# Performance work log

Hardware: AMD Instinct MI355X
Metric: run time of the kernel (lower is better)

## Reference

```python
import jax, jax.numpy as jnp
import numpy as np

B, T, D_MODEL, HEADS = 2, 2048, 1024, 16
D_HEAD = D_MODEL // HEADS


def setup_inputs() -> dict:
    key = jax.random.key(0)
    ks = jax.random.split(key, 9)
    s = 1.0 / np.sqrt(D_HEAD)
    return {
        "x": jax.random.normal(ks[0], (B, T, D_MODEL), dtype=jnp.float32),
        "Wq": jax.random.normal(ks[1], (D_HEAD, D_HEAD), dtype=jnp.float32) * s,
        "bq": jax.random.normal(ks[2], (D_HEAD,), dtype=jnp.float32) * 0.01,
        "Wk": jax.random.normal(ks[3], (D_HEAD, D_HEAD), dtype=jnp.float32) * s,
        "bk": jax.random.normal(ks[4], (D_HEAD,), dtype=jnp.float32) * 0.01,
        "Wv": jax.random.normal(ks[5], (D_HEAD, D_HEAD), dtype=jnp.float32) * s,
        "bv": jax.random.normal(ks[6], (D_HEAD,), dtype=jnp.float32) * 0.01,
        "Wp": jax.random.normal(ks[7], (D_MODEL, D_MODEL), dtype=jnp.float32) * (1.0 / np.sqrt(D_MODEL)),
        "bp": jax.random.normal(ks[8], (D_MODEL,), dtype=jnp.float32) * 0.01,
    }


def reference(x, Wq, bq, Wk, bk, Wv, bv, Wp, bp):
    b, t, c = x.shape
    xh = x.reshape(b, t, HEADS, D_HEAD)  # [B,T,H,dh]
    # per-head linear projections (weights shared across heads), nn.Linear: y = x @ W.T + b
    q = jnp.einsum('bthd,ed->bhte', xh, Wq) + bq  # [B,H,T,dh]
    k = jnp.einsum('bthd,ed->bhte', xh, Wk) + bk
    v = jnp.einsum('bthd,ed->bhte', xh, Wv) + bv
    # NOTE: original scales by sqrt(C) = sqrt(d_model), not sqrt(d_head)
    scale = 1.0 / jnp.sqrt(jnp.float32(c))
    att = jnp.einsum('bhqd,bhkd->bhqk', q, k) * scale  # [B,H,T,T]
    att = jax.nn.softmax(att, axis=-1)
    out = jnp.einsum('bhqk,bhkd->bhqd', att, v)  # [B,H,T,dh]
    out = out.transpose(0, 2, 1, 3).reshape(b, t, c)  # [B,T,C]
    out = out @ Wp.T + bp
    return out
```

## Files before the change

kernel.cpp:

```cpp
#include <hip/hip_runtime.h>
#include <hip/hip_bf16.h>

#define B_ 2
#define T_ 2048
#define DM_ 1024
#define H_ 16
#define DH_ 64
#define QSCALE 0.045084220027780106f

typedef unsigned short u16;
typedef unsigned int u32;
typedef __attribute__((ext_vector_type(2))) unsigned int u32x2;
typedef __attribute__((ext_vector_type(4))) unsigned int u32x4;
typedef __attribute__((ext_vector_type(4))) float f32x4v;
typedef __attribute__((ext_vector_type(8))) short bf16x8;
typedef __attribute__((ext_vector_type(4))) float f32x4;

__device__ __forceinline__ u16 f2bf(float f) {
    u32 u = __float_as_uint(f);
    return (u16)((u + 0x7FFF + ((u >> 16) & 1)) >> 16);
}
__device__ __forceinline__ float bf2f(u16 h) {
    return __uint_as_float(((u32)h) << 16);
}
__device__ __forceinline__ float exp2_fast(float x) {
    float r;
    asm("v_exp_f32 %0, %1" : "=v"(r) : "v"(x));
    return r;
}
__device__ __forceinline__ u32 cvtpk_bf16(float lo, float hi) {
    u32 r;
    asm("v_cvt_pk_bf16_f32 %0, %1, %2" : "=v"(r) : "v"(lo), "v"(hi));
    return r;
}

__device__ __forceinline__ const bf16x8* frag_at(const u16* base, int row, int c16) {
    return (const bf16x8*)((const char*)base + row * 128 + ((c16 ^ (row & 7)) << 4));
}

__global__ __launch_bounds__(256) void wsplit3_kernel(
    const float* __restrict__ Wq, const float* __restrict__ Wk,
    const float* __restrict__ Wv, u16* __restrict__ W6)
{
    const int i = blockIdx.x * 256 + threadIdx.x;
    const int mat = i >> 12, idx = i & 4095;
    const float w = (mat == 0) ? Wq[idx] : (mat == 1) ? Wk[idx] : Wv[idx];
    const u16 hi = f2bf(w);
    W6[(mat * 2) * 4096 + idx] = hi;
    W6[(mat * 2 + 1) * 4096 + idx] = f2bf(w - bf2f(hi));
}

__global__ __launch_bounds__(256) void qkv_mfma(
    const float* __restrict__ x,
    const float* __restrict__ bq, const float* __restrict__ bk,
    const float* __restrict__ bv, const u16* __restrict__ W6,
    u16* __restrict__ Q, u16* __restrict__ K, u16* __restrict__ VT)
{
    __shared__ u16 Ws[6 * 4096];

    const int tid = threadIdx.x;
    const int wid = tid >> 6;
    const int lane = tid & 63;
    const int li = lane & 15, g = lane >> 4;

    const int bh = blockIdx.x >> 4;
    const int t0 = (blockIdx.x & 15) * 128;
    const int b = bh >> 4, h = bh & 15;
    const int tw0 = t0 + wid * 32;

    #pragma unroll
    for (int j = 0; j < 12; ++j) {
        const int gi = j * 256 + tid;
        const int tile = gi >> 9;
        const int t16 = gi & 511;
        const int r = t16 >> 3, c16 = t16 & 7;
        const int c16s = c16 ^ (r & 7);
        __builtin_amdgcn_global_load_lds(
            (const __attribute__((address_space(1))) u32*)((const char*)W6 + tile * 8192 + r * 128 + (c16s << 4)),
            (__attribute__((address_space(3))) u32*)((char*)Ws + gi * 16),
            16, 0, 0);
    }

    const float* xb = x + ((size_t)b * T_) * DM_ + h * 64;
    f32x4v xr[2][2][2];
    #pragma unroll
    for (int mt = 0; mt < 2; ++mt)
        #pragma unroll
        for (int kt = 0; kt < 2; ++kt) {
            const float* p = xb + (size_t)(tw0 + 16 * mt + li) * DM_ + kt * 32 + g * 8;
            xr[mt][kt][0] = *(const f32x4v*)p;
            xr[mt][kt][1] = *(const f32x4v*)(p + 4);
        }

    float bq_r[4], bk_r[4], bv_r[4][4];
    #pragma unroll
    for (int nt = 0; nt < 4; ++nt) { bq_r[nt] = bq[16 * nt + li]; bk_r[nt] = bk[16 * nt + li]; }
    #pragma unroll
    for (int vd = 0; vd < 4; ++vd)
        #pragma unroll
        for (int rg = 0; rg < 4; ++rg) bv_r[vd][rg] = bv[16 * vd + 4 * g + rg];

    __syncthreads();

    bf16x8 xhf[2][2], xlf[2][2];
    #pragma unroll
    for (int mt = 0; mt < 2; ++mt)
        #pragma unroll
        for (int kt = 0; kt < 2; ++kt) {
            u32 hw[4], lw[4];
            #pragma unroll
            for (int q2 = 0; q2 < 2; ++q2) {
                const f32x4v v = xr[mt][kt][q2];
                const u32 p0 = cvtpk_bf16(v[0], v[1]);
                const u32 p1 = cvtpk_bf16(v[2], v[3]);
                const float l0 = v[0] - __uint_as_float(p0 << 16);
                const float l1 = v[1] - __uint_as_float(p0 & 0xFFFF0000u);
                const float l2 = v[2] - __uint_as_float(p1 << 16);
                const float l3 = v[3] - __uint_as_float(p1 & 0xFFFF0000u);
                hw[q2 * 2] = p0; hw[q2 * 2 + 1] = p1;
                lw[q2 * 2] = cvtpk_bf16(l0, l1);
                lw[q2 * 2 + 1] = cvtpk_bf16(l2, l3);
            }
            xhf[mt][kt] = *(const bf16x8*)hw;
            xlf[mt][kt] = *(const bf16x8*)lw;
        }

    const u16* Wqh = Ws;
    const u16* Wql = Ws + 4096;
    const u16* Wkh = Ws + 8192;
    const u16* Wkl = Ws + 12288;
    const u16* Wvh = Ws + 16384;
    const u16* Wvl = Ws + 20480;

    const size_t qk_base = ((size_t)bh * T_) * DH_;

    {
        f32x4 acc[2][4];
        #pragma unroll
        for (int mt = 0; mt < 2; ++mt)
            #pragma unroll
            for (int nt = 0; nt < 4; ++nt) acc[mt][nt] = (f32x4){0.f, 0.f, 0.f, 0.f};
        #pragma unroll
        for (int nt = 0; nt < 4; ++nt)
            #pragma unroll
            for (int kt = 0; kt < 2; ++kt) {
                const bf16x8 wh = *frag_at(Wqh, 16 * nt + li, 4 * kt + g);
                const bf16x8 wl = *frag_at(Wql, 16 * nt + li, 4 * kt + g);
                #pragma unroll
                for (int mt = 0; mt < 2; ++mt) {
                    acc[mt][nt] = __builtin_amdgcn_mfma_f32_16x16x32_bf16(xhf[mt][kt], wh, acc[mt][nt], 0, 0, 0);
                    acc[mt][nt] = __builtin_amdgcn_mfma_f32_16x16x32_bf16(xlf[mt][kt], wh, acc[mt][nt], 0, 0, 0);
                    acc[mt][nt] = __builtin_amdgcn_mfma_f32_16x16x32_bf16(xhf[mt][kt], wl, acc[mt][nt], 0, 0, 0);
                }
            }
        #pragma unroll
        for (int mt = 0; mt < 2; ++mt)
            #pragma unroll
            for (int rg = 0; rg < 4; ++rg) {
                const int t = tw0 + 16 * mt + 4 * g + rg;
                #pragma unroll
                for (int nt = 0; nt < 4; ++nt)
                    Q[qk_base + (size_t)t * DH_ + 16 * nt + li] =
                        f2bf((acc[mt][nt][rg] + bq_r[nt]) * QSCALE);
            }
    }

    {
        f32x4 acc[2][4];
        #pragma unroll
        for (int mt = 0; mt < 2; ++mt)
            #pragma unroll
            for (int nt = 0; nt < 4; ++nt) acc[mt][nt] = (f32x4){0.f, 0.f, 0.f, 0.f};
        #pragma unroll
        for (int nt = 0; nt < 4; ++nt)
            #pragma unroll
            for (int kt = 0; kt < 2; ++kt) {
                const bf16x8 wh = *frag_at(Wkh, 16 * nt + li, 4 * kt + g);
                const bf16x8 wl = *frag_at(Wkl, 16 * nt + li, 4 * kt + g);
                #pragma unroll
                for (int mt = 0; mt < 2; ++mt) {
                    acc[mt][nt] = __builtin_amdgcn_mfma_f32_16x16x32_bf16(xhf[mt][kt], wh, acc[mt][nt], 0, 0, 0);
                    acc[mt][nt] = __builtin_amdgcn_mfma_f32_16x16x32_bf16(xlf[mt][kt], wh, acc[mt][nt], 0, 0, 0);
                    acc[mt][nt] = __builtin_amdgcn_mfma_f32_16x16x32_bf16(xhf[mt][kt], wl, acc[mt][nt], 0, 0, 0);
                }
            }
        #pragma unroll
        for (int mt = 0; mt < 2; ++mt)
            #pragma unroll
            for (int rg = 0; rg < 4; ++rg) {
                const int t = tw0 + 16 * mt + 4 * g + rg;
                #pragma unroll
                for (int nt = 0; nt < 4; ++nt)
                    K[qk_base + (size_t)t * DH_ + 16 * nt + li] =
                        f2bf(acc[mt][nt][rg] + bk_r[nt]);
            }
    }

    {
        f32x4 acc[4][2];
        #pragma unroll
        for (int vd = 0; vd < 4; ++vd)
            #pragma unroll
            for (int tc = 0; tc < 2; ++tc) acc[vd][tc] = (f32x4){0.f, 0.f, 0.f, 0.f};
        #pragma unroll
        for (int vd = 0; vd < 4; ++vd)
            #pragma unroll
            for (int kt = 0; kt < 2; ++kt) {
                const bf16x8 ah = *frag_at(Wvh, 16 * vd + li, 4 * kt + g);
                const bf16x8 al = *frag_at(Wvl, 16 * vd + li, 4 * kt + g);
                #pragma unroll
                for (int tc = 0; tc < 2; ++tc) {
                    acc[vd][tc] = __builtin_amdgcn_mfma_f32_16x16x32_bf16(ah, xhf[tc][kt], acc[vd][tc], 0, 0, 0);
                    acc[vd][tc] = __builtin_amdgcn_mfma_f32_16x16x32_bf16(al, xhf[tc][kt], acc[vd][tc], 0, 0, 0);
                    acc[vd][tc] = __builtin_amdgcn_mfma_f32_16x16x32_bf16(ah, xlf[tc][kt], acc[vd][tc], 0, 0, 0);
                }
            }
        u16* VTb = VT + (size_t)bh * DH_ * T_;
        #pragma unroll
        for (int vd = 0; vd < 4; ++vd)
            #pragma unroll
            for (int rg = 0; rg < 4; ++rg) {
                const int d = 16 * vd + 4 * g + rg;
                #pragma unroll
                for (int tc = 0; tc < 2; ++tc)
                    VTb[(size_t)d * T_ + tw0 + 16 * tc + li] =
                        f2bf(acc[vd][tc][rg] + bv_r[vd][rg]);
            }
    }
}

__global__ __launch_bounds__(512) void attn_mfma(
    const u16* __restrict__ Q, const u16* __restrict__ K,
    const u16* __restrict__ VT, u16* __restrict__ Ah, u16* __restrict__ Al)
{
    __shared__ char smem[49152];

    const int tid = threadIdx.x;
    const int wid = tid >> 6;
    const int lane = tid & 63;
    const int li = lane & 15, g = lane >> 4;
    const int bh = blockIdx.y;
    const int q0 = blockIdx.x * 128 + wid * 16;

    const size_t bhoff = (size_t)bh * T_ * DH_;

    bf16x8 qf[2];
    {
        const u16* Qp = Q + bhoff + (size_t)q0 * DH_;
        #pragma unroll
        for (int kt = 0; kt < 2; ++kt)
            qf[kt] = *(const bf16x8*)(Qp + li * DH_ + kt * 32 + g * 8);
    }

    f32x4 o[4];
    float l_part = 0.f;
    #pragma unroll
    for (int dt = 0; dt < 4; ++dt) o[dt] = (f32x4){0.f, 0.f, 0.f, 0.f};

    const int swk = li & 7;
    const char* ldsA[2];
    #pragma unroll
    for (int kt = 0; kt < 2; ++kt)
        ldsA[kt] = smem + li * 128 + (((4 * kt + g) ^ swk) << 4);
    const char* ldsPr[2];
    #pragma unroll
    for (int kt = 0; kt < 2; ++kt)
        ldsPr[kt] = smem + 32768 + wid * 2048 + li * 128 + (((4 * kt + g) ^ swk) << 4);
    char* ldsPw[4];
    #pragma unroll
    for (int ct = 0; ct < 4; ++ct)
        ldsPw[ct] = smem + 32768 + wid * 2048 + li * 128 + ((32 * ct + 8 * g) ^ (swk << 4));

    const int sl_r = lane >> 3;
    const int sl_c = (lane & 7) ^ sl_r;
    const char* kgp = (const char*)(K + bhoff) + wid * 1024 + sl_r * 128 + (sl_c << 4);
    const char* vgp = (const char*)(VT + (size_t)bh * DH_ * T_) + wid * (8 * T_ * 2) + sl_r * (T_ * 2) + (sl_c << 4);

#define STAGE(BUF)                                                                      \
    {                                                                                   \
        __builtin_amdgcn_global_load_lds(                                               \
            (const __attribute__((address_space(1))) u32*)kgp,                          \
            (__attribute__((address_space(3))) u32*)(smem + (BUF) + wid * 1024),        \
            16, 0, 0);                                                                  \
        __builtin_amdgcn_global_load_lds(                                               \
            (const __attribute__((address_space(1))) u32*)vgp,                          \
            (__attribute__((address_space(3))) u32*)(smem + 16384 + (BUF) + wid * 1024),\
            16, 0, 0);                                                                  \
        kgp += 8192; vgp += 128;                                                        \
    }

#define ATTN_ITER(BUF, PREFBUF, DO_PREF)                                                \
    {                                                                                   \
        __syncthreads();                                                                \
        if (DO_PREF) STAGE(PREFBUF);                                                    \
        f32x4 s[4];                                                                     \
        _Pragma("unroll")                                                               \
        for (int ct = 0; ct < 4; ++ct) s[ct] = (f32x4){0.f, 0.f, 0.f, 0.f};             \
        __builtin_amdgcn_s_setprio(1);                                                  \
        _Pragma("unroll")                                                               \
        for (int ct = 0; ct < 4; ++ct) {                                                \
            _Pragma("unroll")                                                           \
            for (int kt = 0; kt < 2; ++kt) {                                            \
                const bf16x8 kf = *(const bf16x8*)(ldsA[kt] + (BUF) + 2048 * ct);       \
                s[ct] = __builtin_amdgcn_mfma_f32_16x16x32_bf16(kf, qf[kt], s[ct], 0, 0, 0); \
            }                                                                           \
        }                                                                               \
        __builtin_amdgcn_s_setprio(0);                                                  \
        float lacc = 0.f;                                                               \
        _Pragma("unroll")                                                               \
        for (int ct = 0; ct < 4; ++ct) {                                                \
            const float p0 = exp2_fast(s[ct][0]);                                       \
            const float p1 = exp2_fast(s[ct][1]);                                       \
            const float p2 = exp2_fast(s[ct][2]);                                       \
            const float p3 = exp2_fast(s[ct][3]);                                       \
            lacc += (p0 + p1) + (p2 + p3);                                              \
            u32x2 w;                                                                    \
            w.x = cvtpk_bf16(p0, p1);                                                   \
            w.y = cvtpk_bf16(p2, p3);                                                   \
            *(u32x2*)ldsPw[ct] = w;                                                     \
        }                                                                               \
        l_part += lacc;                                                                 \
        __builtin_amdgcn_s_setprio(1);                                                  \
        _Pragma("unroll")                                                               \
        for (int kt = 0; kt < 2; ++kt) {                                                \
            const bf16x8 pf = *(const bf16x8*)ldsPr[kt];                                \
            _Pragma("unroll")                                                           \
            for (int dt = 0; dt < 4; ++dt) {                                            \
                const bf16x8 vf = *(const bf16x8*)(ldsA[kt] + 16384 + (BUF) + 2048 * dt); \
                o[dt] = __builtin_amdgcn_mfma_f32_16x16x32_bf16(vf, pf, o[dt], 0, 0, 0); \
            }                                                                           \
        }                                                                               \
        __builtin_amdgcn_s_setprio(0);                                                  \
    }

    STAGE(0);
    for (int kv = 0; kv < T_ / 64; kv += 2) {
        ATTN_ITER(0, 8192, true);
        ATTN_ITER(8192, 0, (kv + 2 < T_ / 64));
    }
#undef ATTN_ITER
#undef STAGE

    float lt = l_part;
    lt += __shfl_xor(lt, 16);
    lt += __shfl_xor(lt, 32);
    const float inv = 1.0f / lt;

    __syncthreads();

    char* ehi = smem + wid * 4096;
    char* elo = ehi + 2048;
    #pragma unroll
    for (int dt = 0; dt < 4; ++dt) {
        const float v0 = o[dt][0] * inv;
        const float v1 = o[dt][1] * inv;
        const float v2 = o[dt][2] * inv;
        const float v3 = o[dt][3] * inv;
        u32x2 wh, wl;
        wh.x = cvtpk_bf16(v0, v1);
        wh.y = cvtpk_bf16(v2, v3);
        const float l0 = v0 - __uint_as_float(wh.x << 16);
        const float l1 = v1 - __uint_as_float(wh.x & 0xFFFF0000u);
        const float l2 = v2 - __uint_as_float(wh.y << 16);
        const float l3 = v3 - __uint_as_float(wh.y & 0xFFFF0000u);
        wl.x = cvtpk_bf16(l0, l1);
        wl.y = cvtpk_bf16(l2, l3);
        const int byteoff = li * 128 + ((32 * dt + 8 * g) ^ (swk << 4));
        *(u32x2*)(ehi + byteoff) = wh;
        *(u32x2*)(elo + byteoff) = wl;
    }

    const int b = bh >> 4, h = bh & 15;
    const int sub = lane & 7;
    const int row8 = lane >> 3;
    #pragma unroll
    for (int rr = 0; rr < 2; ++rr) {
        const int row = 8 * rr + row8;
        const int byteoff = row * 128 + ((sub ^ row8) << 4);
        const size_t gidx = ((size_t)b * T_ + q0 + row) * DM_ + h * 64 + sub * 8;
        *(u32x4*)(Ah + gidx) = *(const u32x4*)(ehi + byteoff);
        *(u32x4*)(Al + gidx) = *(const u32x4*)(elo + byteoff);
    }
}

__global__ __launch_bounds__(256) void wsplit_kernel(
    const float* __restrict__ W, u16* __restrict__ Wh, u16* __restrict__ Wl)
{
    const int i = blockIdx.x * 256 + threadIdx.x;
    const float w = W[i];
    const u16 hi = f2bf(w);
    Wh[i] = hi;
    Wl[i] = f2bf(w - bf2f(hi));
}

__global__ __launch_bounds__(256) void proj_mfma(
    const u16* __restrict__ Ah, const u16* __restrict__ Al,
    const u16* __restrict__ Wh, const u16* __restrict__ Wl,
    const float* __restrict__ bp, float* __restrict__ out)
{
    __shared__ u16 Ahs[128 * 64], Als[128 * 64], Whs[128 * 64], Wls[128 * 64];

    const int tid = threadIdx.x;
    const int wid = tid >> 6;
    const int lane = tid & 63;
    const int li = lane & 15, g = lane >> 4;
    const int row0 = blockIdx.y * 128, col0 = blockIdx.x * 128;
    const int wr = wid >> 1, wc = wid & 1;

    const char* gbase;
    char* lbase;
    if (wid == 0)      { gbase = (const char*)(Ah + (size_t)row0 * DM_); lbase = (char*)Ahs; }
    else if (wid == 1) { gbase = (const char*)(Al + (size_t)row0 * DM_); lbase = (char*)Als; }
    else if (wid == 2) { gbase = (const char*)(Wh + (size_t)col0 * DM_); lbase = (char*)Whs; }
    else               { gbase = (const char*)(Wl + (size_t)col0 * DM_); lbase = (char*)Wls; }

    f32x4 acc[4][4];
    #pragma unroll
    for (int m = 0; m < 4; ++m)
        #pragma unroll
        for (int n = 0; n < 4; ++n) acc[m][n] = (f32x4){0.f, 0.f, 0.f, 0.f};

    for (int step = 0; step < DM_ / 64; ++step) {
        __syncthreads();
        #pragma unroll
        for (int j = 0; j < 16; ++j) {
            const int gidx = j * 64 + lane;
            const int r = gidx >> 3;
            const int c16s = (gidx & 7) ^ (r & 7);
            __builtin_amdgcn_global_load_lds(
                (const __attribute__((address_space(1))) u32*)(gbase + (size_t)r * (DM_ * 2) + step * 128 + (c16s << 4)),
                (__attribute__((address_space(3))) u32*)(lbase + j * 1024),
                16, 0, 0);
        }
        __syncthreads();

        #pragma unroll
        for (int kt = 0; kt < 2; ++kt) {
            bf16x8 ah[4], al[4], wh[4], wl[4];
            #pragma unroll
            for (int m = 0; m < 4; ++m) {
                ah[m] = *frag_at(Ahs, wr * 64 + m * 16 + li, kt * 4 + g);
                al[m] = *frag_at(Als, wr * 64 + m * 16 + li, kt * 4 + g);
            }
            #pragma unroll
            for (int n = 0; n < 4; ++n) {
                wh[n] = *frag_at(Whs, wc * 64 + n * 16 + li, kt * 4 + g);
                wl[n] = *frag_at(Wls, wc * 64 + n * 16 + li, kt * 4 + g);
            }
            #pragma unroll
            for (int m = 0; m < 4; ++m)
                #pragma unroll
                for (int n = 0; n < 4; ++n) {
                    acc[m][n] = __builtin_amdgcn_mfma_f32_16x16x32_bf16(ah[m], wh[n], acc[m][n], 0, 0, 0);
                    acc[m][n] = __builtin_amdgcn_mfma_f32_16x16x32_bf16(al[m], wh[n], acc[m][n], 0, 0, 0);
                    acc[m][n] = __builtin_amdgcn_mfma_f32_16x16x32_bf16(ah[m], wl[n], acc[m][n], 0, 0, 0);
                }
        }
    }

    const int orow = row0 + wr * 64;
    const int ocol = col0 + wc * 64;
    float bias[4];
    #pragma unroll
    for (int n = 0; n < 4; ++n) bias[n] = bp[ocol + n * 16 + li];
    #pragma unroll
    for (int m = 0; m < 4; ++m)
        #pragma unroll
        for (int n = 0; n < 4; ++n)
            #pragma unroll
            for (int q = 0; q < 4; ++q)
                out[(size_t)(orow + m * 16 + g * 4 + q) * DM_ + ocol + n * 16 + li] =
                    acc[m][n][q] + bias[n];
}

extern "C" void kernel_launch(void* const* d_in, const int* in_sizes, int n_in,
                              void* d_out, int out_size, void* d_ws, size_t ws_size,
                              hipStream_t stream) {
    const float* x  = (const float*)d_in[0];
    const float* Wq = (const float*)d_in[1];
    const float* bq = (const float*)d_in[2];
    const float* Wk = (const float*)d_in[3];
    const float* bk = (const float*)d_in[4];
    const float* Wv = (const float*)d_in[5];
    const float* bv = (const float*)d_in[6];
    const float* Wp = (const float*)d_in[7];
    const float* bp = (const float*)d_in[8];
    float* out = (float*)d_out;

    const size_t n_qkv = (size_t)B_ * H_ * T_ * DH_;
    const size_t n_w   = (size_t)DM_ * DM_;
    u16* Qb  = (u16*)d_ws;
    u16* Kb  = Qb + n_qkv;
    u16* VTb = Kb + n_qkv;
    u16* Ahb = VTb + n_qkv;
    u16* Alb = Ahb + n_qkv;
    u16* Whb = Alb + n_qkv;
    u16* Wlb = Whb + n_w;
    u16* W6b = Wlb + n_w;

    wsplit3_kernel<<<48, 256, 0, stream>>>(Wq, Wk, Wv, W6b);
    wsplit_kernel<<<n_w / 256, 256, 0, stream>>>(Wp, Whb, Wlb);
    qkv_mfma<<<32 * 16, 256, 0, stream>>>(x, bq, bk, bv, W6b, Qb, Kb, VTb);
    attn_mfma<<<dim3(T_ / 128, B_ * H_), 512, 0, stream>>>(Qb, Kb, VTb, Ahb, Alb);
    proj_mfma<<<dim3(DM_ / 128, (B_ * T_) / 128), 256, 0, stream>>>(Ahb, Alb, Whb, Wlb, bp, out);
}
```

Before: 102.9 us.

## Double-buffer proj GEMM with 512 threads, merge weight-split kernels, remap attention grid

The projection GEMM moves to 512 threads with a 128KB double-buffered LDS stage, so the next K-slice loads while MFMAs run, and it raises wave priority around the math. The two weight-split kernels merge into one launch to save launch overhead. The attention grid becomes 1D with a remapped block-to-(bh, q-tile) order so that co-scheduled blocks share K/V for locality. Using 128KB of LDS limits occupancy to one block per CU.

```diff
diff --git a/kernel.cpp b/kernel.cpp
--- a/kernel.cpp
+++ b/kernel.cpp
@@ -38,16 +38,25 @@
     return (const bf16x8*)((const char*)base + row * 128 + ((c16 ^ (row & 7)) << 4));
 }
 
-__global__ __launch_bounds__(256) void wsplit3_kernel(
+__global__ __launch_bounds__(256) void wsplit_all(
     const float* __restrict__ Wq, const float* __restrict__ Wk,
-    const float* __restrict__ Wv, u16* __restrict__ W6)
+    const float* __restrict__ Wv, const float* __restrict__ Wp,
+    u16* __restrict__ W6, u16* __restrict__ Wh, u16* __restrict__ Wl)
 {
     const int i = blockIdx.x * 256 + threadIdx.x;
-    const int mat = i >> 12, idx = i & 4095;
-    const float w = (mat == 0) ? Wq[idx] : (mat == 1) ? Wk[idx] : Wv[idx];
-    const u16 hi = f2bf(w);
-    W6[(mat * 2) * 4096 + idx] = hi;
-    W6[(mat * 2 + 1) * 4096 + idx] = f2bf(w - bf2f(hi));
+    if (i < DM_ * DM_) {
+        const float w = Wp[i];
+        const u16 hi = f2bf(w);
+        Wh[i] = hi;
+        Wl[i] = f2bf(w - bf2f(hi));
+    } else {
+        const int j = i - DM_ * DM_;
+        const int mat = j >> 12, idx = j & 4095;
+        const float w = (mat == 0) ? Wq[idx] : (mat == 1) ? Wk[idx] : Wv[idx];
+        const u16 hi = f2bf(w);
+        W6[(mat * 2) * 4096 + idx] = hi;
+        W6[(mat * 2 + 1) * 4096 + idx] = f2bf(w - bf2f(hi));
+    }
 }
 
 __global__ __launch_bounds__(256) void qkv_mfma(
@@ -239,8 +248,10 @@
     const int wid = tid >> 6;
     const int lane = tid & 63;
     const int li = lane & 15, g = lane >> 4;
-    const int bh = blockIdx.y;
-    const int q0 = blockIdx.x * 128 + wid * 16;
+    const int flat = blockIdx.x;
+    const int bh = (flat & 7) + ((flat >> 7) << 3);
+    const int qx = (flat >> 3) & 15;
+    const int q0 = qx * 128 + wid * 16;
 
     const size_t bhoff = (size_t)bh * T_ * DH_;
 
@@ -383,72 +394,76 @@
     }
 }
 
-__global__ __launch_bounds__(256) void wsplit_kernel(
-    const float* __restrict__ W, u16* __restrict__ Wh, u16* __restrict__ Wl)
-{
-    const int i = blockIdx.x * 256 + threadIdx.x;
-    const float w = W[i];
-    const u16 hi = f2bf(w);
-    Wh[i] = hi;
-    Wl[i] = f2bf(w - bf2f(hi));
-}
-
-__global__ __launch_bounds__(256) void proj_mfma(
+__global__ __launch_bounds__(512) void proj_mfma(
     const u16* __restrict__ Ah, const u16* __restrict__ Al,
     const u16* __restrict__ Wh, const u16* __restrict__ Wl,
     const float* __restrict__ bp, float* __restrict__ out)
 {
-    __shared__ u16 Ahs[128 * 64], Als[128 * 64], Whs[128 * 64], Wls[128 * 64];
+    __shared__ char smem[131072];
 
     const int tid = threadIdx.x;
     const int wid = tid >> 6;
     const int lane = tid & 63;
     const int li = lane & 15, g = lane >> 4;
     const int row0 = blockIdx.y * 128, col0 = blockIdx.x * 128;
+
+    const int mat = wid >> 1, half = wid & 1;
+    const char* gsrc;
+    if (mat == 0)      gsrc = (const char*)(Ah + (size_t)row0 * DM_);
+    else if (mat == 1) gsrc = (const char*)(Al + (size_t)row0 * DM_);
+    else if (mat == 2) gsrc = (const char*)(Wh + (size_t)col0 * DM_);
+    else               gsrc = (const char*)(Wl + (size_t)col0 * DM_);
+    const int r_local = half * 64 + (lane >> 3);
+    const int c16s = (lane & 7) ^ (lane >> 3);
+    const char* gp0 = gsrc + (size_t)r_local * (DM_ * 2) + (c16s << 4);
+    const int ldst0 = mat * 16384 + half * 8192;
+
+#define PSTAGE(BUF, STEP)                                                                \
+    {                                                                                    \
+        _Pragma("unroll")                                                                \
+        for (int j = 0; j < 8; ++j) {                                                    \
+            __builtin_amdgcn_global_load_lds(                                            \
+                (const __attribute__((address_space(1))) u32*)(gp0 + (size_t)(STEP) * 128 + (size_t)j * (8 * DM_ * 2)), \
+                (__attribute__((address_space(3))) u32*)(smem + (BUF) + ldst0 + j * 1024),\
+                16, 0, 0);                                                               \
+        }                                                                                \
+    }
+
     const int wr = wid >> 1, wc = wid & 1;
 
-    const char* gbase;
-    char* lbase;
-    if (wid == 0)      { gbase = (const char*)(Ah + (size_t)row0 * DM_); lbase = (char*)Ahs; }
-    else if (wid == 1) { gbase = (const char*)(Al + (size_t)row0 * DM_); lbase = (char*)Als; }
-    else if (wid == 2) { gbase = (const char*)(Wh + (size_t)col0 * DM_); lbase = (char*)Whs; }
-    else               { gbase = (const char*)(Wl + (size_t)col0 * DM_); lbase = (char*)Wls; }
-
-    f32x4 acc[4][4];
-    #pragma unroll
-    for (int m = 0; m < 4; ++m)
+    f32x4 acc[2][4];
+    #pragma unroll
+    for (int m = 0; m < 2; ++m)
         #pragma unroll
         for (int n = 0; n < 4; ++n) acc[m][n] = (f32x4){0.f, 0.f, 0.f, 0.f};
 
-    for (int step = 0; step < DM_ / 64; ++step) {
+    PSTAGE(0, 0);
+    for (int step = 0; step < 16; ++step) {
+        const int buf = (step & 1) * 65536;
         __syncthreads();
-        #pragma unroll
-        for (int j = 0; j < 16; ++j) {
-            const int gidx = j * 64 + lane;
-            const int r = gidx >> 3;
-            const int c16s = (gidx & 7) ^ (r & 7);
-            __builtin_amdgcn_global_load_lds(
-                (const __attribute__((address_space(1))) u32*)(gbase + (size_t)r * (DM_ * 2) + step * 128 + (c16s << 4)),
-                (__attribute__((address_space(3))) u32*)(lbase + j * 1024),
-                16, 0, 0);
-        }
-        __syncthreads();
-
+        if (step < 15) PSTAGE(buf ^ 65536, step + 1);
+
+        const u16* pAh = (const u16*)(smem + buf);
+        const u16* pAl = (const u16*)(smem + buf + 16384);
+        const u16* pWh = (const u16*)(smem + buf + 32768);
+        const u16* pWl = (const u16*)(smem + buf + 49152);
+
+        __builtin_amdgcn_s_setprio(1);
         #pragma unroll
         for (int kt = 0; kt < 2; ++kt) {
-            bf16x8 ah[4], al[4], wh[4], wl[4];
-            #pragma unroll
-            for (int m = 0; m < 4; ++m) {
-                ah[m] = *frag_at(Ahs, wr * 64 + m * 16 + li, kt * 4 + g);
-                al[m] = *frag_at(Als, wr * 64 + m * 16 + li, kt * 4 + g);
+            bf16x8 ah[2], al[2], wh[4], wl[4];
+            #pragma unroll
+            for (int m = 0; m < 2; ++m) {
+                ah[m] = *frag_at(pAh, wr * 32 + m * 16 + li, kt * 4 + g);
+                al[m] = *frag_at(pAl, wr * 32 + m * 16 + li, kt * 4 + g);
             }
             #pragma unroll
             for (int n = 0; n < 4; ++n) {
-                wh[n] = *frag_at(Whs, wc * 64 + n * 16 + li, kt * 4 + g);
-                wl[n] = *frag_at(Wls, wc * 64 + n * 16 + li, kt * 4 + g);
-            }
-            #pragma unroll
-            for (int m = 0; m < 4; ++m)
+                wh[n] = *frag_at(pWh, wc * 64 + n * 16 + li, kt * 4 + g);
+                wl[n] = *frag_at(pWl, wc * 64 + n * 16 + li, kt * 4 + g);
+            }
+            #pragma unroll
+            for (int m = 0; m < 2; ++m)
                 #pragma unroll
                 for (int n = 0; n < 4; ++n) {
                     acc[m][n] = __builtin_amdgcn_mfma_f32_16x16x32_bf16(ah[m], wh[n], acc[m][n], 0, 0, 0);
@@ -456,15 +471,17 @@
                     acc[m][n] = __builtin_amdgcn_mfma_f32_16x16x32_bf16(ah[m], wl[n], acc[m][n], 0, 0, 0);
                 }
         }
-    }
-
-    const int orow = row0 + wr * 64;
+        __builtin_amdgcn_s_setprio(0);
+    }
+#undef PSTAGE
+
+    const int orow = row0 + wr * 32;
     const int ocol = col0 + wc * 64;
     float bias[4];
     #pragma unroll
     for (int n = 0; n < 4; ++n) bias[n] = bp[ocol + n * 16 + li];
     #pragma unroll
-    for (int m = 0; m < 4; ++m)
+    for (int m = 0; m < 2; ++m)
         #pragma unroll
         for (int n = 0; n < 4; ++n)
             #pragma unroll
@@ -498,9 +515,8 @@
     u16* Wlb = Whb + n_w;
     u16* W6b = Wlb + n_w;
 
-    wsplit3_kernel<<<48, 256, 0, stream>>>(Wq, Wk, Wv, W6b);
-    wsplit_kernel<<<n_w / 256, 256, 0, stream>>>(Wp, Whb, Wlb);
+    wsplit_all<<<(n_w + 12288) / 256, 256, 0, stream>>>(Wq, Wk, Wv, Wp, W6b, Whb, Wlb);
     qkv_mfma<<<32 * 16, 256, 0, stream>>>(x, bq, bk, bv, W6b, Qb, Kb, VTb);
-    attn_mfma<<<dim3(T_ / 128, B_ * H_), 512, 0, stream>>>(Qb, Kb, VTb, Ahb, Alb);
-    proj_mfma<<<dim3(DM_ / 128, (B_ * T_) / 128), 256, 0, stream>>>(Ahb, Alb, Whb, Wlb, bp, out);
-}
+    attn_mfma<<<512, 512, 0, stream>>>(Qb, Kb, VTb, Ahb, Alb);
+    proj_mfma<<<dim3(DM_ / 128, (B_ * T_) / 128), 512, 0, stream>>>(Ahb, Alb, Whb, Wlb, bp, out);
+}
```

Measured after the change: 90.39 us. 1.14x faster.
